# Kernel optimization log

Measured on AMD Instinct MI355X. Metric: run time of the kernel, lower is better.

Reference implementation:

```python
import jax, jax.numpy as jnp
import numpy as np

SOFTCAP = 50.0  # GEMMA2_TANH_SCALE
N_HEADS = 16

def _rope(x, cos, sin):
    # x: [B,S,H,D]; cos/sin: [S,D/2]; interleaved complex pairs as in apply_rotary_emb
    x0 = x[..., 0::2]
    x1 = x[..., 1::2]
    c = cos[None, :, None, :]
    s = sin[None, :, None, :]
    r0 = x0 * c - x1 * s
    r1 = x0 * s + x1 * c
    return jnp.stack([r0, r1], axis=-1).reshape(x.shape)

def setup_inputs() -> dict:
    key = jax.random.key(0)
    ks = jax.random.split(key, 5)
    B, S, DM = 1, 2048, 2048
    hd = DM // N_HEADS
    scale = 1.0 / np.sqrt(DM)
    x = jax.random.normal(ks[0], (B, S, DM), jnp.float32)
    wq = jax.random.normal(ks[1], (DM, DM), jnp.float32) * scale
    wk = jax.random.normal(ks[2], (DM, DM), jnp.float32) * scale
    wv = jax.random.normal(ks[3], (DM, DM), jnp.float32) * scale
    wo = jax.random.normal(ks[4], (DM, DM), jnp.float32) * scale
    # rotary tables, theta=10000 as in llama
    inv_freq = 10000.0 ** (-jnp.arange(0, hd, 2, dtype=jnp.float32) / hd)
    ang = jnp.arange(S, dtype=jnp.float32)[:, None] * inv_freq[None, :]
    return {"x": x, "wq": wq, "wk": wk, "wv": wv, "wo": wo,
            "freqs_cos": jnp.cos(ang), "freqs_sin": jnp.sin(ang)}

def reference(x, wq, wk, wv, wo, freqs_cos, freqs_sin):
    B, S, DM = x.shape
    H = N_HEADS
    hd = DM // H
    q = (x @ wq).reshape(B, S, H, hd)
    k = (x @ wk).reshape(B, S, H, hd)
    v = (x @ wv).reshape(B, S, H, hd)
    q = _rope(q, freqs_cos, freqs_sin)
    k = _rope(k, freqs_cos, freqs_sin)
    # scores [B,H,S,S]
    scores = jnp.einsum('bqhd,bkhd->bhqk', q, k) / jnp.sqrt(jnp.float32(hd))
    scores = SOFTCAP * jnp.tanh(scores / SOFTCAP)  # gemma2 tanh soft-cap
    causal = jnp.tril(jnp.ones((S, S), dtype=bool))
    scores = jnp.where(causal[None, None], scores, -jnp.inf)
    p = jax.nn.softmax(scores, axis=-1)
    o = jnp.einsum('bhqk,bkhd->bqhd', p, v).reshape(B, S, DM)
    return o @ wo
```

## Files before the change

### kernel.cpp

```cpp
#include <hip/hip_runtime.h>
#include <hip/hip_bf16.h>

typedef __attribute__((ext_vector_type(8))) short short8;
typedef __attribute__((ext_vector_type(4))) short short4v;
typedef __attribute__((ext_vector_type(4))) float f32x4;
typedef __attribute__((ext_vector_type(4))) float float4v;

#define S_LEN 2048
#define DMODEL 2048
#define N_HEADS 16
#define HEAD_DIM 128

__device__ __forceinline__ float bf2f(__hip_bfloat16 b) { return __bfloat162float(b); }
__device__ __forceinline__ __hip_bfloat16 f2bf(float f) { return __float2bfloat16(f); }
__device__ __forceinline__ short bfs(float f) {
    union { __hip_bfloat16 b; short s; } x; x.b = __float2bfloat16(f); return x.s;
}
__device__ __forceinline__ float sbf(short s) {
    union { short s; __hip_bfloat16 b; } x; x.s = s; return __bfloat162float(x.b);
}

#if __has_builtin(__builtin_amdgcn_global_load_lds)
#define HAVE_ASYNC_LDS 1
#else
#define HAVE_ASYNC_LDS 0
#endif

__device__ __forceinline__ void stage16(const __hip_bfloat16* g, __hip_bfloat16* ldsbase, int lane) {
#if HAVE_ASYNC_LDS
    __builtin_amdgcn_global_load_lds(
        (const __attribute__((address_space(1))) unsigned int*)g,
        (__attribute__((address_space(3))) unsigned int*)ldsbase,
        16, 0, 0);
#else
    *(short8*)((char*)ldsbase + lane * 16) = *(const short8*)g;
#endif
}

__global__ __launch_bounds__(256) void prep(const float* __restrict__ x,
                                            const float* __restrict__ w0,
                                            const float* __restrict__ w1,
                                            const float* __restrict__ w2,
                                            const float* __restrict__ w3,
                                            __hip_bfloat16* __restrict__ xb,
                                            __hip_bfloat16* __restrict__ o0,
                                            __hip_bfloat16* __restrict__ o1,
                                            __hip_bfloat16* __restrict__ o2,
                                            __hip_bfloat16* __restrict__ o3) {
    const int z = blockIdx.z;
    const int tid = threadIdx.x;
    if (z == 4) {
        size_t base = (((size_t)blockIdx.y * 32 + blockIdx.x) * 256 + tid) * 16;
        for (int i = 0; i < 4; ++i) {
            float4v v = *(const float4v*)(x + base + i * 4);
            short4v p;
            p.x = bfs(v.x); p.y = bfs(v.y); p.z = bfs(v.z); p.w = bfs(v.w);
            *(short4v*)((short*)xb + base + i * 4) = p;
        }
        return;
    }
    const float* in = (z == 0) ? w0 : (z == 1) ? w1 : (z == 2) ? w2 : w3;
    __hip_bfloat16* out = (z == 0) ? o0 : (z == 1) ? o1 : (z == 2) ? o2 : o3;
    __shared__ short tile[64][68];
    const int bx = blockIdx.x * 64;
    const int by = blockIdx.y * 64;
    const int c4 = (tid & 15) * 4;
    for (int rr = 0; rr < 4; ++rr) {
        int r = (tid >> 4) + rr * 16;
        float4v v = *(const float4v*)(in + (size_t)(by + r) * DMODEL + bx + c4);
        short4v p;
        p.x = bfs(v.x); p.y = bfs(v.y); p.z = bfs(v.z); p.w = bfs(v.w);
        *(short4v*)&tile[r][c4] = p;
    }
    __syncthreads();
    const int oc = tid >> 2;
    const int s0 = (tid & 3) * 16;
    short8 a, b;
    for (int i = 0; i < 8; ++i) ((short*)&a)[i] = tile[s0 + i][oc];
    for (int i = 0; i < 8; ++i) ((short*)&b)[i] = tile[s0 + 8 + i][oc];
    *(short8*)((short*)out + (size_t)(bx + oc) * DMODEL + by + s0) = a;
    *(short8*)((short*)out + (size_t)(bx + oc) * DMODEL + by + s0 + 8) = b;
}

__global__ __launch_bounds__(256) void gemm_qkv_sk(const __hip_bfloat16* __restrict__ A,
                                                   const __hip_bfloat16* __restrict__ Bq,
                                                   const __hip_bfloat16* __restrict__ Bk,
                                                   const __hip_bfloat16* __restrict__ Bv,
                                                   __hip_bfloat16* __restrict__ Q0,
                                                   __hip_bfloat16* __restrict__ Q1,
                                                   __hip_bfloat16* __restrict__ K0,
                                                   __hip_bfloat16* __restrict__ K1,
                                                   __hip_bfloat16* __restrict__ V0t,
                                                   __hip_bfloat16* __restrict__ V1t) {
    __shared__ alignas(16) __hip_bfloat16 As[128 * 32];
    __shared__ alignas(16) __hip_bfloat16 Bs[128 * 32];
    const int bx = blockIdx.x;
    const int which = bx >> 5;
    const int kh = (bx >> 4) & 1;
    const __hip_bfloat16* Bt = (which == 0) ? Bq : (which == 1) ? Bk : Bv;
    const int tid = threadIdx.x;
    const int wave = tid >> 6;
    const int lane = tid & 63;
    const int lane15 = lane & 15;
    const int quad = lane >> 4;
    const int m0 = blockIdx.y * 128;
    const int n0 = (bx & 15) * 128;
    const int wm = (wave >> 1) * 64;
    const int wn = (wave & 1) * 64;

    f32x4 acc[4][4];
    for (int i = 0; i < 4; ++i)
        for (int j = 0; j < 4; ++j)
            acc[i][j] = {0.f, 0.f, 0.f, 0.f};

    const int rA = lane >> 2;
    const int cA = (lane & 3) * 8;
    const int kbeg = kh * 1024;

    for (int k0 = kbeg; k0 < kbeg + 1024; k0 += 32) {
        __syncthreads();
        for (int c = 0; c < 4; ++c) {
            int chunk = wave * 4 + c;
            if (chunk < 8) {
                int r = chunk * 16 + rA;
                stage16(A + (size_t)(m0 + r) * DMODEL + k0 + cA, As + chunk * 512, lane);
            } else {
                int r = (chunk - 8) * 16 + rA;
                stage16(Bt + (size_t)(n0 + r) * DMODEL + k0 + cA, Bs + (chunk - 8) * 512, lane);
            }
        }
#if HAVE_ASYNC_LDS
        asm volatile("s_waitcnt vmcnt(0)" ::: "memory");
#endif
        __syncthreads();

        short8 af[4], bfr[4];
        for (int mt = 0; mt < 4; ++mt)
            af[mt] = *(const short8*)(As + (wm + mt * 16 + lane15) * 32 + quad * 8);
        for (int nt = 0; nt < 4; ++nt)
            bfr[nt] = *(const short8*)(Bs + (wn + nt * 16 + lane15) * 32 + quad * 8);
        for (int mt = 0; mt < 4; ++mt)
            for (int nt = 0; nt < 4; ++nt)
                acc[mt][nt] = __builtin_amdgcn_mfma_f32_16x16x32_bf16(af[mt], bfr[nt], acc[mt][nt], 0, 0, 0);
    }

    if (which < 2) {
        __hip_bfloat16* C = (which == 0) ? (kh ? Q1 : Q0) : (kh ? K1 : K0);
        for (int mt = 0; mt < 4; ++mt)
            for (int nt = 0; nt < 4; ++nt)
                for (int i = 0; i < 4; ++i) {
                    int row = m0 + wm + mt * 16 + quad * 4 + i;
                    int col = n0 + wn + nt * 16 + lane15;
                    C[(size_t)row * DMODEL + col] = f2bf(acc[mt][nt][i]);
                }
    } else {
        __hip_bfloat16* Vp = kh ? V1t : V0t;
        for (int mt = 0; mt < 4; ++mt) {
            int rowbase = m0 + wm + mt * 16 + quad * 4;
            for (int nt = 0; nt < 4; ++nt) {
                int col = n0 + wn + nt * 16 + lane15;
                short4v pk;
                pk.x = bfs(acc[mt][nt][0]);
                pk.y = bfs(acc[mt][nt][1]);
                pk.z = bfs(acc[mt][nt][2]);
                pk.w = bfs(acc[mt][nt][3]);
                *(short4v*)((short*)Vp + (size_t)col * S_LEN + rowbase) = pk;
            }
        }
    }
}

__global__ __launch_bounds__(256) void reduce_rope(__hip_bfloat16* __restrict__ Q0,
                                                   const __hip_bfloat16* __restrict__ Q1,
                                                   __hip_bfloat16* __restrict__ K0,
                                                   const __hip_bfloat16* __restrict__ K1,
                                                   __hip_bfloat16* __restrict__ V0,
                                                   const __hip_bfloat16* __restrict__ V1,
                                                   const float* __restrict__ fc,
                                                   const float* __restrict__ fs) {
    const int z = blockIdx.z;
    __hip_bfloat16* P0 = (z == 0) ? Q0 : (z == 1) ? K0 : V0;
    const __hip_bfloat16* P1 = (z == 0) ? Q1 : (z == 1) ? K1 : V1;
    size_t i0 = ((size_t)blockIdx.x * 256 + threadIdx.x) * 8;
    short8 a = *(const short8*)((const short*)P0 + i0);
    short8 b = *(const short8*)((const short*)P1 + i0);
    float s[8];
    for (int i = 0; i < 8; ++i) s[i] = sbf(((short*)&a)[i]) + sbf(((short*)&b)[i]);
    short8 o;
    if (z < 2) {
        int row = (int)(i0 >> 11);
        int col = (int)(i0 & 2047);
        int j0 = (col & 127) >> 1;
        for (int p = 0; p < 4; ++p) {
            float c = fc[row * 64 + j0 + p];
            float sn = fs[row * 64 + j0 + p];
            float e = s[2 * p], od = s[2 * p + 1];
            ((short*)&o)[2 * p]     = bfs(e * c - od * sn);
            ((short*)&o)[2 * p + 1] = bfs(e * sn + od * c);
        }
    } else {
        for (int i = 0; i < 8; ++i) ((short*)&o)[i] = bfs(s[i]);
    }
    *(short8*)((short*)P0 + i0) = o;
}

__global__ __launch_bounds__(256) void gemm_qkv_fused(const __hip_bfloat16* __restrict__ A,
                                                      const __hip_bfloat16* __restrict__ Bq,
                                                      const __hip_bfloat16* __restrict__ Bk,
                                                      const __hip_bfloat16* __restrict__ Bv,
                                                      __hip_bfloat16* __restrict__ Cq,
                                                      __hip_bfloat16* __restrict__ Ck,
                                                      __hip_bfloat16* __restrict__ Cvt,
                                                      const float* __restrict__ fc,
                                                      const float* __restrict__ fs) {
    __shared__ alignas(16) __hip_bfloat16 As[2][128 * 32];
    __shared__ alignas(16) __hip_bfloat16 Bs[2][128 * 32];
    const int which = blockIdx.x >> 4;
    const __hip_bfloat16* Bt = (which == 0) ? Bq : (which == 1) ? Bk : Bv;
    const int tid = threadIdx.x;
    const int wave = tid >> 6;
    const int lane = tid & 63;
    const int lane15 = lane & 15;
    const int quad = lane >> 4;
    const int m0 = blockIdx.y * 128;
    const int n0 = (blockIdx.x & 15) * 128;
    const int wm = (wave >> 1) * 64;
    const int wn = (wave & 1) * 64;
    f32x4 acc[4][4];
    for (int i = 0; i < 4; ++i)
        for (int j = 0; j < 4; ++j)
            acc[i][j] = {0.f, 0.f, 0.f, 0.f};
    const int rA = lane >> 2;
    const int cA = (lane & 3) * 8;
    for (int k0 = 0; k0 < DMODEL; k0 += 64) {
        __syncthreads();
        for (int h = 0; h < 2; ++h) {
            int kk = k0 + h * 32;
            for (int c = 0; c < 4; ++c) {
                int chunk = wave * 4 + c;
                if (chunk < 8) {
                    int r = chunk * 16 + rA;
                    stage16(A + (size_t)(m0 + r) * DMODEL + kk + cA, As[h] + chunk * 512, lane);
                } else {
                    int r = (chunk - 8) * 16 + rA;
                    stage16(Bt + (size_t)(n0 + r) * DMODEL + kk + cA, Bs[h] + (chunk - 8) * 512, lane);
                }
            }
        }
#if HAVE_ASYNC_LDS
        asm volatile("s_waitcnt vmcnt(0)" ::: "memory");
#endif
        __syncthreads();
        for (int h = 0; h < 2; ++h) {
            short8 af[4], bfr[4];
            for (int mt = 0; mt < 4; ++mt)
                af[mt] = *(const short8*)(As[h] + (wm + mt * 16 + lane15) * 32 + quad * 8);
            for (int nt = 0; nt < 4; ++nt)
                bfr[nt] = *(const short8*)(Bs[h] + (wn + nt * 16 + lane15) * 32 + quad * 8);
            for (int mt = 0; mt < 4; ++mt)
                for (int nt = 0; nt < 4; ++nt)
                    acc[mt][nt] = __builtin_amdgcn_mfma_f32_16x16x32_bf16(af[mt], bfr[nt], acc[mt][nt], 0, 0, 0);
        }
    }
    if (which < 2) {
        __hip_bfloat16* C = (which == 0) ? Cq : Ck;
        for (int mt = 0; mt < 4; ++mt)
            for (int nt = 0; nt < 4; ++nt) {
                int col = n0 + wn + nt * 16 + lane15;
                int j = (col & 127) >> 1;
                bool odd = col & 1;
                for (int i = 0; i < 4; ++i) {
                    int row = m0 + wm + mt * 16 + quad * 4 + i;
                    float v = acc[mt][nt][i];
                    float p = __shfl_xor(v, 1, 64);
                    float c = fc[row * 64 + j];
                    float sn = fs[row * 64 + j];
                    float r = odd ? (p * sn + v * c) : (v * c - p * sn);
                    C[(size_t)row * DMODEL + col] = f2bf(r);
                }
            }
    } else {
        for (int mt = 0; mt < 4; ++mt) {
            int rowbase = m0 + wm + mt * 16 + quad * 4;
            for (int nt = 0; nt < 4; ++nt) {
                int col = n0 + wn + nt * 16 + lane15;
                short4v pk;
                pk.x = bfs(acc[mt][nt][0]);
                pk.y = bfs(acc[mt][nt][1]);
                pk.z = bfs(acc[mt][nt][2]);
                pk.w = bfs(acc[mt][nt][3]);
                *(short4v*)((short*)Cvt + (size_t)col * S_LEN + rowbase) = pk;
            }
        }
    }
}

__global__ __launch_bounds__(256) void gemm_out(const __hip_bfloat16* __restrict__ A,
                                                const __hip_bfloat16* __restrict__ Bt,
                                                float* __restrict__ C) {
    __shared__ alignas(16) __hip_bfloat16 As[2][128 * 32];
    __shared__ alignas(16) __hip_bfloat16 Bs[2][64 * 32];
    const int tid = threadIdx.x;
    const int wave = tid >> 6;
    const int lane = tid & 63;
    const int lane15 = lane & 15;
    const int quad = lane >> 4;
    const int m0 = blockIdx.y * 128;
    const int n0 = blockIdx.x * 64;
    const int wm = (wave >> 1) * 64;
    const int wn = (wave & 1) * 32;
    f32x4 acc[4][2];
    for (int i = 0; i < 4; ++i)
        for (int j = 0; j < 2; ++j)
            acc[i][j] = {0.f, 0.f, 0.f, 0.f};
    const int rA = lane >> 2;
    const int cA = (lane & 3) * 8;
    for (int k0 = 0; k0 < DMODEL; k0 += 64) {
        __syncthreads();
        for (int h = 0; h < 2; ++h) {
            int kk = k0 + h * 32;
            for (int c = 0; c < 3; ++c) {
                int chunk = wave * 3 + c;
                if (chunk < 8) {
                    int r = chunk * 16 + rA;
                    stage16(A + (size_t)(m0 + r) * DMODEL + kk + cA, As[h] + chunk * 512, lane);
                } else {
                    int r = (chunk - 8) * 16 + rA;
                    stage16(Bt + (size_t)(n0 + r) * DMODEL + kk + cA, Bs[h] + (chunk - 8) * 512, lane);
                }
            }
        }
#if HAVE_ASYNC_LDS
        asm volatile("s_waitcnt vmcnt(0)" ::: "memory");
#endif
        __syncthreads();
        for (int h = 0; h < 2; ++h) {
            short8 af[4], bfr[2];
            for (int mt = 0; mt < 4; ++mt)
                af[mt] = *(const short8*)(As[h] + (wm + mt * 16 + lane15) * 32 + quad * 8);
            for (int nt = 0; nt < 2; ++nt)
                bfr[nt] = *(const short8*)(Bs[h] + (wn + nt * 16 + lane15) * 32 + quad * 8);
            for (int mt = 0; mt < 4; ++mt)
                for (int nt = 0; nt < 2; ++nt)
                    acc[mt][nt] = __builtin_amdgcn_mfma_f32_16x16x32_bf16(af[mt], bfr[nt], acc[mt][nt], 0, 0, 0);
        }
    }
    for (int mt = 0; mt < 4; ++mt)
        for (int nt = 0; nt < 2; ++nt)
            for (int i = 0; i < 4; ++i) {
                int row = m0 + wm + mt * 16 + quad * 4 + i;
                int col = n0 + wn + nt * 16 + lane15;
                C[(size_t)row * DMODEL + col] = acc[mt][nt][i];
            }
}

__global__ __launch_bounds__(256) void flash_attn(const __hip_bfloat16* __restrict__ Q,
                                                  const __hip_bfloat16* __restrict__ Kb,
                                                  const __hip_bfloat16* __restrict__ Vt,
                                                  __hip_bfloat16* __restrict__ O) {
    __shared__ alignas(16) short Ks[32][136];
    __shared__ alignas(16) short Vs[128][40];
    __shared__ alignas(16) short Pl[4][16][40];
    const int tid = threadIdx.x;
    const int wave = tid >> 6;
    const int lane = tid & 63;
    const int lane15 = lane & 15;
    const int quad = lane >> 4;
    const int bx = blockIdx.x;
    const int u = bx & 255;
    const int head = u & 15;
    const int qp = u >> 4;
    const int qb = (bx < 256) ? (31 - qp) : qp;
    const int qbase = qb * 64;
    const int q0w = qbase + wave * 16;
    const int nkt = 2 * qb + 2;
    const float K1 = 0.08838834764831845f * (1.0f / 25.0f);

    const __hip_bfloat16* Qh = Q + (size_t)q0w * DMODEL + head * HEAD_DIM;
    short8 qf[4];
    for (int kk = 0; kk < 4; ++kk)
        qf[kk] = *(const short8*)(Qh + (size_t)lane15 * DMODEL + kk * 32 + quad * 8);

    f32x4 acc[8];
    for (int i = 0; i < 8; ++i) acc[i] = {0.f, 0.f, 0.f, 0.f};
    float lpart[4] = {0.f, 0.f, 0.f, 0.f};

    const int krow = tid >> 3, kcol = (tid & 7) * 16;
    const int vrow = tid >> 1, vcol = (tid & 1) * 16;
    const __hip_bfloat16* Kg = Kb + (size_t)krow * DMODEL + head * HEAD_DIM + kcol;
    const __hip_bfloat16* Vg = Vt + (size_t)(head * HEAD_DIM + vrow) * S_LEN + vcol;

    short8 gk0 = *(const short8*)(Kg);
    short8 gk1 = *(const short8*)(Kg + 8);
    short8 gv0 = *(const short8*)(Vg);
    short8 gv1 = *(const short8*)(Vg + 8);

    for (int kt = 0; kt < nkt; ++kt) {
        const int kb = kt * 32;
        __syncthreads();
        *(short8*)&Ks[krow][kcol] = gk0;
        *(short8*)&Ks[krow][kcol + 8] = gk1;
        *(short8*)&Vs[vrow][vcol] = gv0;
        *(short8*)&Vs[vrow][vcol + 8] = gv1;
        __syncthreads();

        if (kt + 1 < nkt) {
            const __hip_bfloat16* Kg2 = Kg + (size_t)(kb + 32) * DMODEL;
            const __hip_bfloat16* Vg2 = Vg + kb + 32;
            gk0 = *(const short8*)(Kg2);
            gk1 = *(const short8*)(Kg2 + 8);
            gv0 = *(const short8*)(Vg2);
            gv1 = *(const short8*)(Vg2 + 8);
        }

        if (kb <= q0w + 15) {
            f32x4 sc[2];
            sc[0] = {0.f, 0.f, 0.f, 0.f};
            sc[1] = {0.f, 0.f, 0.f, 0.f};
            for (int c = 0; c < 2; ++c)
                for (int kk = 0; kk < 4; ++kk) {
                    short8 kf = *(const short8*)&Ks[c * 16 + lane15][kk * 32 + quad * 8];
                    sc[c] = __builtin_amdgcn_mfma_f32_16x16x32_bf16(qf[kk], kf, sc[c], 0, 0, 0);
                }

            const bool masked = (kb + 31 > q0w);
            const int key0 = kb + lane15;
            const int key1 = kb + 16 + lane15;
            for (int i = 0; i < 4; ++i) {
                float e0 = __expf(sc[0][i] * K1);
                float e1 = __expf(sc[1][i] * K1);
                float c0 = __builtin_fmaf(-100.0f, __builtin_amdgcn_rcpf(e0 + 1.0f), 40.0f);
                float c1 = __builtin_fmaf(-100.0f, __builtin_amdgcn_rcpf(e1 + 1.0f), 40.0f);
                float p0 = __expf(c0);
                float p1 = __expf(c1);
                if (masked) {
                    int q = q0w + quad * 4 + i;
                    if (key0 > q) p0 = 0.f;
                    if (key1 > q) p1 = 0.f;
                }
                short b0 = bfs(p0), b1 = bfs(p1);
                lpart[i] += sbf(b0) + sbf(b1);
                Pl[wave][quad * 4 + i][lane15] = b0;
                Pl[wave][quad * 4 + i][16 + lane15] = b1;
            }
            asm volatile("s_waitcnt lgkmcnt(0)" ::: "memory");
            short8 pf = *(const short8*)&Pl[wave][lane15][quad * 8];
            asm volatile("" ::: "memory");
            for (int nt = 0; nt < 8; ++nt) {
                short8 vf = *(const short8*)&Vs[nt * 16 + lane15][quad * 8];
                acc[nt] = __builtin_amdgcn_mfma_f32_16x16x32_bf16(pf, vf, acc[nt], 0, 0, 0);
            }
        }
    }

    for (int i = 0; i < 4; ++i) {
        float l = lpart[i];
        l += __shfl_xor(l, 1, 64);
        l += __shfl_xor(l, 2, 64);
        l += __shfl_xor(l, 4, 64);
        l += __shfl_xor(l, 8, 64);
        float inv = 1.0f / l;
        int row = q0w + quad * 4 + i;
        for (int nt = 0; nt < 8; ++nt) {
            int col = head * HEAD_DIM + nt * 16 + lane15;
            O[(size_t)row * DMODEL + col] = f2bf(acc[nt][i] * inv);
        }
    }
}

extern "C" void kernel_launch(void* const* d_in, const int* in_sizes, int n_in,
                              void* d_out, int out_size, void* d_ws, size_t ws_size,
                              hipStream_t stream) {
    const float* x  = (const float*)d_in[0];
    const float* wq = (const float*)d_in[1];
    const float* wk = (const float*)d_in[2];
    const float* wv = (const float*)d_in[3];
    const float* wo = (const float*)d_in[4];
    const float* fc = (const float*)d_in[5];
    const float* fs = (const float*)d_in[6];
    float* out = (float*)d_out;

    char* ws = (char*)d_ws;
    const size_t MB8 = (size_t)2048 * 2048 * sizeof(__hip_bfloat16);
    __hip_bfloat16* wq_t = (__hip_bfloat16*)(ws + 0 * MB8);
    __hip_bfloat16* wk_t = (__hip_bfloat16*)(ws + 1 * MB8);
    __hip_bfloat16* wv_t = (__hip_bfloat16*)(ws + 2 * MB8);
    __hip_bfloat16* wo_t = (__hip_bfloat16*)(ws + 3 * MB8);
    __hip_bfloat16* s4   = (__hip_bfloat16*)(ws + 4 * MB8);
    __hip_bfloat16* s5   = (__hip_bfloat16*)(ws + 5 * MB8);
    __hip_bfloat16* s6   = (__hip_bfloat16*)(ws + 6 * MB8);
    __hip_bfloat16* s7   = (__hip_bfloat16*)(ws + 7 * MB8);
    __hip_bfloat16* s8   = (__hip_bfloat16*)(ws + 8 * MB8);
    __hip_bfloat16* s9   = (__hip_bfloat16*)(ws + 9 * MB8);
    __hip_bfloat16* x_bf = (__hip_bfloat16*)d_out;

    prep<<<dim3(32, 32, 5), 256, 0, stream>>>(x, wq, wk, wv, wo, x_bf, wq_t, wk_t, wv_t, wo_t);

    if (ws_size >= 10 * MB8) {
        gemm_qkv_sk<<<dim3(96, 16), 256, 0, stream>>>(x_bf, wq_t, wk_t, wv_t,
                                                      s4, s7, s5, s8, s6, s9);
        reduce_rope<<<dim3(2048, 1, 3), 256, 0, stream>>>(s4, s7, s5, s8, s6, s9, fc, fs);
        flash_attn<<<512, 256, 0, stream>>>(s4, s5, s6, wq_t);
        gemm_out<<<dim3(32, 16), 256, 0, stream>>>(wq_t, wo_t, out);
    } else {
        gemm_qkv_fused<<<dim3(48, 16), 256, 0, stream>>>(x_bf, wq_t, wk_t, wv_t,
                                                         s4, s5, s6, fc, fs);
        flash_attn<<<512, 256, 0, stream>>>(s4, s5, s6, wq_t);
        gemm_out<<<dim3(32, 16), 256, 0, stream>>>(wq_t, wo_t, out);
    }
}
```

Baseline: 307.9 us.

## Split attention key range and output GEMM K across blocks with combine kernels

Flash attention now gives each block 128 query rows (two 16-row groups per wave, reusing each staged K/V tile). The causal key range is split into two halves across separate blocks, which write unnormalized fp32 partial outputs and row sums. A new combine kernel sums and normalizes these partials into bf16. The output projection is split along K into two halves with fp32 partials plus an add kernel, and the workspace-size fallback path is removed. The aim is better load balance and occupancy, at the cost of extra fp32 intermediate traffic and two more launches.

```diff
diff --git a/kernel.cpp b/kernel.cpp
--- a/kernel.cpp
+++ b/kernel.cpp
@@ -204,163 +204,15 @@
     *(short8*)((short*)P0 + i0) = o;
 }
 
-__global__ __launch_bounds__(256) void gemm_qkv_fused(const __hip_bfloat16* __restrict__ A,
-                                                      const __hip_bfloat16* __restrict__ Bq,
-                                                      const __hip_bfloat16* __restrict__ Bk,
-                                                      const __hip_bfloat16* __restrict__ Bv,
-                                                      __hip_bfloat16* __restrict__ Cq,
-                                                      __hip_bfloat16* __restrict__ Ck,
-                                                      __hip_bfloat16* __restrict__ Cvt,
-                                                      const float* __restrict__ fc,
-                                                      const float* __restrict__ fs) {
-    __shared__ alignas(16) __hip_bfloat16 As[2][128 * 32];
-    __shared__ alignas(16) __hip_bfloat16 Bs[2][128 * 32];
-    const int which = blockIdx.x >> 4;
-    const __hip_bfloat16* Bt = (which == 0) ? Bq : (which == 1) ? Bk : Bv;
-    const int tid = threadIdx.x;
-    const int wave = tid >> 6;
-    const int lane = tid & 63;
-    const int lane15 = lane & 15;
-    const int quad = lane >> 4;
-    const int m0 = blockIdx.y * 128;
-    const int n0 = (blockIdx.x & 15) * 128;
-    const int wm = (wave >> 1) * 64;
-    const int wn = (wave & 1) * 64;
-    f32x4 acc[4][4];
-    for (int i = 0; i < 4; ++i)
-        for (int j = 0; j < 4; ++j)
-            acc[i][j] = {0.f, 0.f, 0.f, 0.f};
-    const int rA = lane >> 2;
-    const int cA = (lane & 3) * 8;
-    for (int k0 = 0; k0 < DMODEL; k0 += 64) {
-        __syncthreads();
-        for (int h = 0; h < 2; ++h) {
-            int kk = k0 + h * 32;
-            for (int c = 0; c < 4; ++c) {
-                int chunk = wave * 4 + c;
-                if (chunk < 8) {
-                    int r = chunk * 16 + rA;
-                    stage16(A + (size_t)(m0 + r) * DMODEL + kk + cA, As[h] + chunk * 512, lane);
-                } else {
-                    int r = (chunk - 8) * 16 + rA;
-                    stage16(Bt + (size_t)(n0 + r) * DMODEL + kk + cA, Bs[h] + (chunk - 8) * 512, lane);
-                }
-            }
-        }
-#if HAVE_ASYNC_LDS
-        asm volatile("s_waitcnt vmcnt(0)" ::: "memory");
-#endif
-        __syncthreads();
-        for (int h = 0; h < 2; ++h) {
-            short8 af[4], bfr[4];
-            for (int mt = 0; mt < 4; ++mt)
-                af[mt] = *(const short8*)(As[h] + (wm + mt * 16 + lane15) * 32 + quad * 8);
-            for (int nt = 0; nt < 4; ++nt)
-                bfr[nt] = *(const short8*)(Bs[h] + (wn + nt * 16 + lane15) * 32 + quad * 8);
-            for (int mt = 0; mt < 4; ++mt)
-                for (int nt = 0; nt < 4; ++nt)
-                    acc[mt][nt] = __builtin_amdgcn_mfma_f32_16x16x32_bf16(af[mt], bfr[nt], acc[mt][nt], 0, 0, 0);
-        }
-    }
-    if (which < 2) {
-        __hip_bfloat16* C = (which == 0) ? Cq : Ck;
-        for (int mt = 0; mt < 4; ++mt)
-            for (int nt = 0; nt < 4; ++nt) {
-                int col = n0 + wn + nt * 16 + lane15;
-                int j = (col & 127) >> 1;
-                bool odd = col & 1;
-                for (int i = 0; i < 4; ++i) {
-                    int row = m0 + wm + mt * 16 + quad * 4 + i;
-                    float v = acc[mt][nt][i];
-                    float p = __shfl_xor(v, 1, 64);
-                    float c = fc[row * 64 + j];
-                    float sn = fs[row * 64 + j];
-                    float r = odd ? (p * sn + v * c) : (v * c - p * sn);
-                    C[(size_t)row * DMODEL + col] = f2bf(r);
-                }
-            }
-    } else {
-        for (int mt = 0; mt < 4; ++mt) {
-            int rowbase = m0 + wm + mt * 16 + quad * 4;
-            for (int nt = 0; nt < 4; ++nt) {
-                int col = n0 + wn + nt * 16 + lane15;
-                short4v pk;
-                pk.x = bfs(acc[mt][nt][0]);
-                pk.y = bfs(acc[mt][nt][1]);
-                pk.z = bfs(acc[mt][nt][2]);
-                pk.w = bfs(acc[mt][nt][3]);
-                *(short4v*)((short*)Cvt + (size_t)col * S_LEN + rowbase) = pk;
-            }
-        }
-    }
-}
-
-__global__ __launch_bounds__(256) void gemm_out(const __hip_bfloat16* __restrict__ A,
-                                                const __hip_bfloat16* __restrict__ Bt,
-                                                float* __restrict__ C) {
-    __shared__ alignas(16) __hip_bfloat16 As[2][128 * 32];
-    __shared__ alignas(16) __hip_bfloat16 Bs[2][64 * 32];
-    const int tid = threadIdx.x;
-    const int wave = tid >> 6;
-    const int lane = tid & 63;
-    const int lane15 = lane & 15;
-    const int quad = lane >> 4;
-    const int m0 = blockIdx.y * 128;
-    const int n0 = blockIdx.x * 64;
-    const int wm = (wave >> 1) * 64;
-    const int wn = (wave & 1) * 32;
-    f32x4 acc[4][2];
-    for (int i = 0; i < 4; ++i)
-        for (int j = 0; j < 2; ++j)
-            acc[i][j] = {0.f, 0.f, 0.f, 0.f};
-    const int rA = lane >> 2;
-    const int cA = (lane & 3) * 8;
-    for (int k0 = 0; k0 < DMODEL; k0 += 64) {
-        __syncthreads();
-        for (int h = 0; h < 2; ++h) {
-            int kk = k0 + h * 32;
-            for (int c = 0; c < 3; ++c) {
-                int chunk = wave * 3 + c;
-                if (chunk < 8) {
-                    int r = chunk * 16 + rA;
-                    stage16(A + (size_t)(m0 + r) * DMODEL + kk + cA, As[h] + chunk * 512, lane);
-                } else {
-                    int r = (chunk - 8) * 16 + rA;
-                    stage16(Bt + (size_t)(n0 + r) * DMODEL + kk + cA, Bs[h] + (chunk - 8) * 512, lane);
-                }
-            }
-        }
-#if HAVE_ASYNC_LDS
-        asm volatile("s_waitcnt vmcnt(0)" ::: "memory");
-#endif
-        __syncthreads();
-        for (int h = 0; h < 2; ++h) {
-            short8 af[4], bfr[2];
-            for (int mt = 0; mt < 4; ++mt)
-                af[mt] = *(const short8*)(As[h] + (wm + mt * 16 + lane15) * 32 + quad * 8);
-            for (int nt = 0; nt < 2; ++nt)
-                bfr[nt] = *(const short8*)(Bs[h] + (wn + nt * 16 + lane15) * 32 + quad * 8);
-            for (int mt = 0; mt < 4; ++mt)
-                for (int nt = 0; nt < 2; ++nt)
-                    acc[mt][nt] = __builtin_amdgcn_mfma_f32_16x16x32_bf16(af[mt], bfr[nt], acc[mt][nt], 0, 0, 0);
-        }
-    }
-    for (int mt = 0; mt < 4; ++mt)
-        for (int nt = 0; nt < 2; ++nt)
-            for (int i = 0; i < 4; ++i) {
-                int row = m0 + wm + mt * 16 + quad * 4 + i;
-                int col = n0 + wn + nt * 16 + lane15;
-                C[(size_t)row * DMODEL + col] = acc[mt][nt][i];
-            }
-}
-
-__global__ __launch_bounds__(256) void flash_attn(const __hip_bfloat16* __restrict__ Q,
-                                                  const __hip_bfloat16* __restrict__ Kb,
-                                                  const __hip_bfloat16* __restrict__ Vt,
-                                                  __hip_bfloat16* __restrict__ O) {
+__global__ __launch_bounds__(256) void flash_attn_sk(const __hip_bfloat16* __restrict__ Q,
+                                                     const __hip_bfloat16* __restrict__ Kb,
+                                                     const __hip_bfloat16* __restrict__ Vt,
+                                                     float* __restrict__ Of0,
+                                                     float* __restrict__ Of1,
+                                                     float* __restrict__ Lf) {
     __shared__ alignas(16) short Ks[32][136];
     __shared__ alignas(16) short Vs[128][40];
-    __shared__ alignas(16) short Pl[4][16][40];
+    __shared__ alignas(16) short Pl[4][32][40];
     const int tid = threadIdx.x;
     const int wave = tid >> 6;
     const int lane = tid & 63;
@@ -370,32 +222,36 @@
     const int u = bx & 255;
     const int head = u & 15;
     const int qp = u >> 4;
-    const int qb = (bx < 256) ? (31 - qp) : qp;
-    const int qbase = qb * 64;
-    const int q0w = qbase + wave * 16;
-    const int nkt = 2 * qb + 2;
+    const int half = bx >> 8;
+    const int qb = half ? (15 - qp) : qp;
+    const int q0w = qb * 128 + wave * 32;
+    const int t0 = half ? (2 * qb + 2) : 0;
+    const int t1 = half ? (4 * qb + 4) : (2 * qb + 2);
     const float K1 = 0.08838834764831845f * (1.0f / 25.0f);
 
-    const __hip_bfloat16* Qh = Q + (size_t)q0w * DMODEL + head * HEAD_DIM;
-    short8 qf[4];
-    for (int kk = 0; kk < 4; ++kk)
-        qf[kk] = *(const short8*)(Qh + (size_t)lane15 * DMODEL + kk * 32 + quad * 8);
-
-    f32x4 acc[8];
-    for (int i = 0; i < 8; ++i) acc[i] = {0.f, 0.f, 0.f, 0.f};
-    float lpart[4] = {0.f, 0.f, 0.f, 0.f};
+    short8 qf[2][4];
+    for (int rg = 0; rg < 2; ++rg) {
+        const __hip_bfloat16* Qh = Q + (size_t)(q0w + rg * 16) * DMODEL + head * HEAD_DIM;
+        for (int kk = 0; kk < 4; ++kk)
+            qf[rg][kk] = *(const short8*)(Qh + (size_t)lane15 * DMODEL + kk * 32 + quad * 8);
+    }
+
+    f32x4 acc[2][8];
+    for (int rg = 0; rg < 2; ++rg)
+        for (int i = 0; i < 8; ++i) acc[rg][i] = {0.f, 0.f, 0.f, 0.f};
+    float lpart[2][4] = {{0.f, 0.f, 0.f, 0.f}, {0.f, 0.f, 0.f, 0.f}};
 
     const int krow = tid >> 3, kcol = (tid & 7) * 16;
     const int vrow = tid >> 1, vcol = (tid & 1) * 16;
     const __hip_bfloat16* Kg = Kb + (size_t)krow * DMODEL + head * HEAD_DIM + kcol;
     const __hip_bfloat16* Vg = Vt + (size_t)(head * HEAD_DIM + vrow) * S_LEN + vcol;
 
-    short8 gk0 = *(const short8*)(Kg);
-    short8 gk1 = *(const short8*)(Kg + 8);
-    short8 gv0 = *(const short8*)(Vg);
-    short8 gv1 = *(const short8*)(Vg + 8);
-
-    for (int kt = 0; kt < nkt; ++kt) {
+    short8 gk0 = *(const short8*)(Kg + (size_t)(t0 * 32) * DMODEL);
+    short8 gk1 = *(const short8*)(Kg + (size_t)(t0 * 32) * DMODEL + 8);
+    short8 gv0 = *(const short8*)(Vg + t0 * 32);
+    short8 gv1 = *(const short8*)(Vg + t0 * 32 + 8);
+
+    for (int kt = t0; kt < t1; ++kt) {
         const int kb = kt * 32;
         __syncthreads();
         *(short8*)&Ks[krow][kcol] = gk0;
@@ -404,7 +260,7 @@
         *(short8*)&Vs[vrow][vcol + 8] = gv1;
         __syncthreads();
 
-        if (kt + 1 < nkt) {
+        if (kt + 1 < t1) {
             const __hip_bfloat16* Kg2 = Kg + (size_t)(kb + 32) * DMODEL;
             const __hip_bfloat16* Vg2 = Vg + kb + 32;
             gk0 = *(const short8*)(Kg2);
@@ -413,17 +269,20 @@
             gv1 = *(const short8*)(Vg2 + 8);
         }
 
-        if (kb <= q0w + 15) {
+        for (int rg = 0; rg < 2; ++rg) {
+            const int q0r = q0w + rg * 16;
+            if (kb > q0r + 15) continue;
+
             f32x4 sc[2];
             sc[0] = {0.f, 0.f, 0.f, 0.f};
             sc[1] = {0.f, 0.f, 0.f, 0.f};
             for (int c = 0; c < 2; ++c)
                 for (int kk = 0; kk < 4; ++kk) {
                     short8 kf = *(const short8*)&Ks[c * 16 + lane15][kk * 32 + quad * 8];
-                    sc[c] = __builtin_amdgcn_mfma_f32_16x16x32_bf16(qf[kk], kf, sc[c], 0, 0, 0);
+                    sc[c] = __builtin_amdgcn_mfma_f32_16x16x32_bf16(qf[rg][kk], kf, sc[c], 0, 0, 0);
                 }
 
-            const bool masked = (kb + 31 > q0w);
+            const bool masked = (kb + 31 > q0r);
             const int key0 = kb + lane15;
             const int key1 = kb + 16 + lane15;
             for (int i = 0; i < 4; ++i) {
@@ -434,37 +293,130 @@
                 float p0 = __expf(c0);
                 float p1 = __expf(c1);
                 if (masked) {
-                    int q = q0w + quad * 4 + i;
+                    int q = q0r + quad * 4 + i;
                     if (key0 > q) p0 = 0.f;
                     if (key1 > q) p1 = 0.f;
                 }
                 short b0 = bfs(p0), b1 = bfs(p1);
-                lpart[i] += sbf(b0) + sbf(b1);
-                Pl[wave][quad * 4 + i][lane15] = b0;
-                Pl[wave][quad * 4 + i][16 + lane15] = b1;
+                lpart[rg][i] += sbf(b0) + sbf(b1);
+                Pl[wave][rg * 16 + quad * 4 + i][lane15] = b0;
+                Pl[wave][rg * 16 + quad * 4 + i][16 + lane15] = b1;
             }
             asm volatile("s_waitcnt lgkmcnt(0)" ::: "memory");
-            short8 pf = *(const short8*)&Pl[wave][lane15][quad * 8];
+            short8 pf = *(const short8*)&Pl[wave][rg * 16 + lane15][quad * 8];
             asm volatile("" ::: "memory");
             for (int nt = 0; nt < 8; ++nt) {
                 short8 vf = *(const short8*)&Vs[nt * 16 + lane15][quad * 8];
-                acc[nt] = __builtin_amdgcn_mfma_f32_16x16x32_bf16(pf, vf, acc[nt], 0, 0, 0);
-            }
-        }
-    }
-
-    for (int i = 0; i < 4; ++i) {
-        float l = lpart[i];
-        l += __shfl_xor(l, 1, 64);
-        l += __shfl_xor(l, 2, 64);
-        l += __shfl_xor(l, 4, 64);
-        l += __shfl_xor(l, 8, 64);
-        float inv = 1.0f / l;
-        int row = q0w + quad * 4 + i;
-        for (int nt = 0; nt < 8; ++nt) {
-            int col = head * HEAD_DIM + nt * 16 + lane15;
-            O[(size_t)row * DMODEL + col] = f2bf(acc[nt][i] * inv);
-        }
+                acc[rg][nt] = __builtin_amdgcn_mfma_f32_16x16x32_bf16(pf, vf, acc[rg][nt], 0, 0, 0);
+            }
+        }
+    }
+
+    float* Ofh = half ? Of1 : Of0;
+    float* Lfh = Lf + (size_t)half * N_HEADS * S_LEN;
+    for (int rg = 0; rg < 2; ++rg)
+        for (int i = 0; i < 4; ++i) {
+            float l = lpart[rg][i];
+            l += __shfl_xor(l, 1, 64);
+            l += __shfl_xor(l, 2, 64);
+            l += __shfl_xor(l, 4, 64);
+            l += __shfl_xor(l, 8, 64);
+            int row = q0w + rg * 16 + quad * 4 + i;
+            if (lane15 == 0) Lfh[head * S_LEN + row] = l;
+            for (int nt = 0; nt < 8; ++nt) {
+                int col = head * HEAD_DIM + nt * 16 + lane15;
+                Ofh[(size_t)row * DMODEL + col] = acc[rg][nt][i];
+            }
+        }
+}
+
+__global__ __launch_bounds__(256) void combine_attn(const float* __restrict__ Of0,
+                                                    const float* __restrict__ Of1,
+                                                    const float* __restrict__ Lf,
+                                                    __hip_bfloat16* __restrict__ attn) {
+    size_t i0 = ((size_t)blockIdx.x * 256 + threadIdx.x) * 8;
+    int row = (int)(i0 >> 11);
+    int head = ((int)(i0 & 2047)) >> 7;
+    float l = Lf[head * S_LEN + row] + Lf[N_HEADS * S_LEN + head * S_LEN + row];
+    float inv = 1.0f / l;
+    short8 o;
+    for (int i = 0; i < 8; ++i)
+        ((short*)&o)[i] = bfs((Of0[i0 + i] + Of1[i0 + i]) * inv);
+    *(short8*)((short*)attn + i0) = o;
+}
+
+__global__ __launch_bounds__(256) void gemm_out_sk(const __hip_bfloat16* __restrict__ A,
+                                                   const __hip_bfloat16* __restrict__ Bt,
+                                                   float* __restrict__ P0,
+                                                   float* __restrict__ P1) {
+    __shared__ alignas(16) __hip_bfloat16 As[128 * 32];
+    __shared__ alignas(16) __hip_bfloat16 Bs[64 * 32];
+    const int tid = threadIdx.x;
+    const int wave = tid >> 6;
+    const int lane = tid & 63;
+    const int lane15 = lane & 15;
+    const int quad = lane >> 4;
+    const int m0 = blockIdx.y * 128;
+    const int n0 = blockIdx.x * 64;
+    const int wm = (wave >> 1) * 64;
+    const int wn = (wave & 1) * 32;
+    float* P = blockIdx.z ? P1 : P0;
+    const int kbeg = blockIdx.z * 1024;
+
+    f32x4 acc[4][2];
+    for (int i = 0; i < 4; ++i)
+        for (int j = 0; j < 2; ++j)
+            acc[i][j] = {0.f, 0.f, 0.f, 0.f};
+
+    const int rA = lane >> 2;
+    const int cA = (lane & 3) * 8;
+
+    for (int k0 = kbeg; k0 < kbeg + 1024; k0 += 32) {
+        __syncthreads();
+        for (int c = 0; c < 3; ++c) {
+            int chunk = wave * 3 + c;
+            if (chunk < 8) {
+                int r = chunk * 16 + rA;
+                stage16(A + (size_t)(m0 + r) * DMODEL + k0 + cA, As + chunk * 512, lane);
+            } else {
+                int r = (chunk - 8) * 16 + rA;
+                stage16(Bt + (size_t)(n0 + r) * DMODEL + k0 + cA, Bs + (chunk - 8) * 512, lane);
+            }
+        }
+#if HAVE_ASYNC_LDS
+        asm volatile("s_waitcnt vmcnt(0)" ::: "memory");
+#endif
+        __syncthreads();
+
+        short8 af[4], bfr[2];
+        for (int mt = 0; mt < 4; ++mt)
+            af[mt] = *(const short8*)(As + (wm + mt * 16 + lane15) * 32 + quad * 8);
+        for (int nt = 0; nt < 2; ++nt)
+            bfr[nt] = *(const short8*)(Bs + (wn + nt * 16 + lane15) * 32 + quad * 8);
+        for (int mt = 0; mt < 4; ++mt)
+            for (int nt = 0; nt < 2; ++nt)
+                acc[mt][nt] = __builtin_amdgcn_mfma_f32_16x16x32_bf16(af[mt], bfr[nt], acc[mt][nt], 0, 0, 0);
+    }
+
+    for (int mt = 0; mt < 4; ++mt)
+        for (int nt = 0; nt < 2; ++nt)
+            for (int i = 0; i < 4; ++i) {
+                int row = m0 + wm + mt * 16 + quad * 4 + i;
+                int col = n0 + wn + nt * 16 + lane15;
+                P[(size_t)row * DMODEL + col] = acc[mt][nt][i];
+            }
+}
+
+__global__ __launch_bounds__(256) void combine_out(const float* __restrict__ P0,
+                                                   const float* __restrict__ P1,
+                                                   float* __restrict__ out) {
+    size_t i0 = ((size_t)blockIdx.x * 256 + threadIdx.x) * 8;
+    for (int i = 0; i < 8; i += 4) {
+        float4v a = *(const float4v*)(P0 + i0 + i);
+        float4v b = *(const float4v*)(P1 + i0 + i);
+        float4v o;
+        o.x = a.x + b.x; o.y = a.y + b.y; o.z = a.z + b.z; o.w = a.w + b.w;
+        *(float4v*)(out + i0 + i) = o;
     }
 }
 
@@ -496,16 +448,20 @@
 
     prep<<<dim3(32, 32, 5), 256, 0, stream>>>(x, wq, wk, wv, wo, x_bf, wq_t, wk_t, wv_t, wo_t);
 
-    if (ws_size >= 10 * MB8) {
-        gemm_qkv_sk<<<dim3(96, 16), 256, 0, stream>>>(x_bf, wq_t, wk_t, wv_t,
-                                                      s4, s7, s5, s8, s6, s9);
-        reduce_rope<<<dim3(2048, 1, 3), 256, 0, stream>>>(s4, s7, s5, s8, s6, s9, fc, fs);
-        flash_attn<<<512, 256, 0, stream>>>(s4, s5, s6, wq_t);
-        gemm_out<<<dim3(32, 16), 256, 0, stream>>>(wq_t, wo_t, out);
-    } else {
-        gemm_qkv_fused<<<dim3(48, 16), 256, 0, stream>>>(x_bf, wq_t, wk_t, wv_t,
-                                                         s4, s5, s6, fc, fs);
-        flash_attn<<<512, 256, 0, stream>>>(s4, s5, s6, wq_t);
-        gemm_out<<<dim3(32, 16), 256, 0, stream>>>(wq_t, wo_t, out);
-    }
-}
+    gemm_qkv_sk<<<dim3(96, 16), 256, 0, stream>>>(x_bf, wq_t, wk_t, wv_t,
+                                                  s4, s7, s5, s8, s6, s9);
+    reduce_rope<<<dim3(2048, 1, 3), 256, 0, stream>>>(s4, s7, s5, s8, s6, s9, fc, fs);
+
+    float* Of0 = (float*)s7;
+    float* Of1 = (float*)wq_t;
+    float* Lf  = (float*)s9;
+    flash_attn_sk<<<512, 256, 0, stream>>>(s4, s5, s6, Of0, Of1, Lf);
+
+    __hip_bfloat16* attn = wv_t;
+    combine_attn<<<2048, 256, 0, stream>>>(Of0, Of1, Lf, attn);
+
+    float* P0 = (float*)s4;
+    float* P1 = (float*)s6;
+    gemm_out_sk<<<dim3(32, 16, 2), 256, 0, stream>>>(attn, wo_t, P0, P1);
+    combine_out<<<2048, 256, 0, stream>>>(P0, P1, out);
+}
```

New measurement: 309.8 us. Within noise of the previous version (+0.6%).
